# Kernel tuning notes

Hardware: AMD Instinct MI355X
Metric: run time of the kernel (lower is better)

Reference implementation:

```python
import jax, jax.numpy as jnp
import numpy as np

N, K, IN, OUT, H = 20000, 32, 128, 256, 64  # H = OUT // 4 (bottleneck hidden)
EPS = 1e-5

def leaky(x):
    return jnp.where(x >= 0, x, 0.1 * x)

def bn(x, g, b, axes):
    # training-mode batch norm: batch statistics over `axes`, per-channel affine
    m = jnp.mean(x, axis=axes, keepdims=True)
    v = jnp.var(x, axis=axes, keepdims=True)
    return (x - m) * jax.lax.rsqrt(v + EPS) * g + b

def setup_inputs() -> dict:
    key = jax.random.key(0)
    ks = jax.random.split(key, 12)
    q_pts = jax.random.normal(ks[0], (N, 3), jnp.float32)
    return {
        'features': jax.random.normal(ks[1], (N, IN), jnp.float32),
        'q_pts': q_pts,
        's_pts': q_pts,  # non-strided block: queries == supports
        'neighb_inds': jax.random.randint(ks[2], (N, K), 0, N, dtype=jnp.int32),
        'w_unary1': jax.random.normal(ks[3], (IN, H), jnp.float32) * 0.05,
        'g1': jnp.ones(H, jnp.float32), 'b1': jnp.zeros(H, jnp.float32),
        'w_conv0': jax.random.normal(ks[4], (H, H), jnp.float32) * 0.05,
        'g_bn0': jnp.ones(H, jnp.float32), 'b_bn0': jnp.zeros(H, jnp.float32),
        'w_conv1': jax.random.normal(ks[5], (H, H * 3), jnp.float32) * 0.05,
        'g_bn1': jnp.ones(H, jnp.float32), 'b_bn1': jnp.zeros(H, jnp.float32),
        'g_bnc': jnp.ones(H, jnp.float32), 'b_bnc': jnp.zeros(H, jnp.float32),
        'w_unary2': jax.random.normal(ks[6], (H, OUT), jnp.float32) * 0.05,
        'g2': jnp.ones(OUT, jnp.float32), 'b2': jnp.zeros(OUT, jnp.float32),
        'w_sc': jax.random.normal(ks[7], (IN, OUT), jnp.float32) * 0.05,
        'g_sc': jnp.ones(OUT, jnp.float32), 'b_sc': jnp.zeros(OUT, jnp.float32),
    }

def reference(features, q_pts, s_pts, neighb_inds,
              w_unary1, g1, b1,
              w_conv0, g_bn0, b_bn0,
              w_conv1, g_bn1, b_bn1,
              g_bnc, b_bnc,
              w_unary2, g2, b2,
              w_sc, g_sc, b_sc):
    # unary1: Linear -> BN1d -> LeakyReLU
    x = leaky(bn(features @ w_unary1, g1, b1, 0))              # [N, H]
    # pad with zero shadow row (index N = out-of-range neighbor)
    s_pad = jnp.concatenate([s_pts, jnp.zeros((1, 3), s_pts.dtype)], 0)
    f_pad = jnp.concatenate([x, jnp.zeros((1, H), x.dtype)], 0)
    nb_x = s_pad[neighb_inds] - q_pts[:, None, :]              # [N, K, 3]
    nb_y = f_pad[neighb_inds]                                  # [N, K, H]
    # adaptive kernel generation: 1x1 conv -> BN2d -> LeakyReLU -> 1x1 conv
    k0 = leaky(bn(jnp.einsum('nkc,cd->nkd', nb_y, w_conv0), g_bn0, b_bn0, (0, 1)))
    kern = jnp.einsum('nkd,de->nke', k0, w_conv1).reshape(N, K, H, 3)
    # per-neighbor dynamic matmul: [H,3] @ [3] per (n,k)
    msg = jnp.einsum('nkhc,nkc->nkh', kern, nb_x)              # [N, K, H]
    msg = leaky(bn(msg, g_bn1, b_bn1, (0, 1)))
    agg = jnp.max(msg, axis=1)                                 # [N, H] max over neighbors
    # batch_norm_conv + LeakyReLU
    agg = leaky(bn(agg, g_bnc, b_bnc, 0))
    # unary2 (no relu) + shortcut (no relu)
    xo = bn(agg @ w_unary2, g2, b2, 0)                         # [N, OUT]
    sc = bn(features @ w_sc, g_sc, b_sc, 0)                    # [N, OUT]
    return leaky(xo + sc)
```

## Files before the change

kernel.cpp:

```cpp
#include <hip/hip_runtime.h>

#define KNB 32
#define CIN 128
#define CH 64
#define COUT 256
#define BN_EPS 1e-5f
#define CONV_GRID 256

typedef __attribute__((ext_vector_type(8))) short bf16x8;
typedef __attribute__((ext_vector_type(4))) float f32x4;

static __device__ __forceinline__ float leakyf(float v){ return fmaxf(v, 0.1f*v); }

static __device__ __forceinline__ unsigned short f2bf(float f){
    unsigned u = __float_as_uint(f);
    u += 0x7FFFu + ((u >> 16) & 1u);
    return (unsigned short)(u >> 16);
}
static __device__ __forceinline__ float bf2f(ushort u){ return __uint_as_float(((unsigned)u) << 16); }

static __device__ __forceinline__ unsigned cvtpk(float lo, float hi){
    unsigned r;
    asm("v_cvt_pk_bf16_f32 %0, %1, %2" : "=v"(r) : "v"(lo), "v"(hi));
    return r;
}

static __device__ __forceinline__ void bn_affine_wave(const float* __restrict__ G, const float* __restrict__ s,
    const float* __restrict__ W, const float* __restrict__ gg, const float* __restrict__ bb,
    float invcnt, int D, int M, int o, int lane, float& ai, float& ci)
{
    float pm = 0.f, pq = 0.f;
    for (int i = lane; i < D; i += 64){
        float wi = W[i*M + o];
        pm += s[i]*wi;
        float t = 0.f;
        for (int j = 0; j < D; ++j) t += G[i*D + j]*W[j*M + o];
        pq += wi*t;
    }
    #pragma unroll
    for (int off = 32; off; off >>= 1){
        pm += __shfl_down(pm, off);
        pq += __shfl_down(pq, off);
    }
    float m  = pm*invcnt;
    float var = pq*invcnt - m*m;
    float a_ = gg[o]*rsqrtf(var + BN_EPS);
    float c_ = bb[o] - m*a_;
    ai = __shfl(a_, 0);
    ci = __shfl(c_, 0);
}

__global__ __launch_bounds__(512) void k1_kernel(const float* __restrict__ feat, const int* __restrict__ inds,
    const float* __restrict__ W1, int N,
    float* __restrict__ slabA, ushort* __restrict__ featbf, ushort* __restrict__ w1s,
    ushort* __restrict__ xbf, float* __restrict__ cnt)
{
    __shared__ ushort Xt[128][40];
    __shared__ float red[16][128];
    int tid = threadIdx.x, bid = blockIdx.x;
    if (bid < 128){
        int wave = tid >> 6, lane = tid & 63, l15 = lane & 15, g = lane >> 4;
        int wr = wave >> 1, wc = wave & 1;
        const f32x4 z4 = {0.f,0.f,0.f,0.f};
        f32x4 acc[2][4];
        #pragma unroll
        for (int i=0;i<2;++i)
            #pragma unroll
            for (int j=0;j<4;++j) acc[i][j] = z4;
        float pcs[4] = {0,0,0,0};
        int nch = (N + 31) >> 5;
        for (int ch = bid; ch < nch; ch += 128){
            int base = ch << 5;
            __syncthreads();
            #pragma unroll
            for (int ii=0; ii<2; ++ii){
                int i = tid + ii*512;
                int r = i >> 5, c4 = i & 31;
                int n = base + r;
                float4 v = make_float4(0.f,0.f,0.f,0.f);
                if (n < N) v = ((const float4*)feat)[(size_t)n*32 + c4];
                ushort b0=f2bf(v.x), b1=f2bf(v.y), b2=f2bf(v.z), b3=f2bf(v.w);
                Xt[c4*4+0][r]=b0; Xt[c4*4+1][r]=b1; Xt[c4*4+2][r]=b2; Xt[c4*4+3][r]=b3;
                pcs[0]+=bf2f(b0); pcs[1]+=bf2f(b1); pcs[2]+=bf2f(b2); pcs[3]+=bf2f(b3);
            }
            __syncthreads();
            bf16x8 af[2], bv[4];
            #pragma unroll
            for (int t=0;t<2;++t) af[t] = *(const bf16x8*)&Xt[wr*32 + t*16 + l15][g*8];
            #pragma unroll
            for (int u=0;u<4;++u) bv[u] = *(const bf16x8*)&Xt[wc*64 + u*16 + l15][g*8];
            #pragma unroll
            for (int t=0;t<2;++t)
                #pragma unroll
                for (int u=0;u<4;++u)
                    acc[t][u] = __builtin_amdgcn_mfma_f32_16x16x32_bf16(af[t], bv[u], acc[t][u], 0,0,0);
        }
        float* Gp = slabA + (size_t)bid*16512;
        #pragma unroll
        for (int t=0;t<2;++t)
            #pragma unroll
            for (int u=0;u<4;++u)
                #pragma unroll
                for (int q=0;q<4;++q)
                    Gp[(wr*32 + t*16 + g*4 + q)*CIN + wc*64 + u*16 + l15] = acc[t][u][q];
        __syncthreads();
        { int r16 = tid >> 5, c4 = tid & 31;
          #pragma unroll
          for (int j=0;j<4;++j) red[r16][c4*4+j] = pcs[j]; }
        __syncthreads();
        if (tid < CIN){
            float s = 0.f;
            #pragma unroll
            for (int k=0;k<16;++k) s += red[k][tid];
            Gp[16384 + tid] = s;
        }
    } else {
        int t2 = (bid-128)*512 + tid;
        const int TG = 128*512;
        for (int i = t2; i < N*32; i += TG){
            float4 v = ((const float4*)feat)[i];
            uint2 pk; pk.x = cvtpk(v.x, v.y); pk.y = cvtpk(v.z, v.w);
            ((uint2*)featbf)[i] = pk;
        }
        for (int i = t2; i < N*KNB; i += TG){
            int ix = inds[i];
            if ((unsigned)ix < (unsigned)N) atomicAdd(&cnt[ix], 1.0f);
        }
        if (t2 < 192*CH){
            int r = t2 >> 6, dd = t2 & 63;
            int c = r >> 6, h = r & 63;
            w1s[t2] = f2bf(W1[dd*192 + 3*h + c]);
        }
        if (t2 < CH) xbf[(size_t)N*CH + t2] = 0;
    }
}

__global__ __launch_bounds__(256) void reduce_slab(const float* __restrict__ slab, int nparts, int len,
                                                   float* __restrict__ dst)
{
    int j = blockIdx.x*256 + threadIdx.x;
    if (j < len){
        float s0 = 0.f, s1 = 0.f, s2 = 0.f, s3 = 0.f;
        int b = 0;
        for (; b + 4 <= nparts; b += 4){
            s0 += slab[(size_t)(b+0)*len + j];
            s1 += slab[(size_t)(b+1)*len + j];
            s2 += slab[(size_t)(b+2)*len + j];
            s3 += slab[(size_t)(b+3)*len + j];
        }
        for (; b < nparts; ++b) s0 += slab[(size_t)b*len + j];
        dst[j] = (s0 + s1) + (s2 + s3);
    }
}

__global__ __launch_bounds__(512) void k3_finA(const float* __restrict__ XtX, const float* __restrict__ fsum,
    const float* __restrict__ Wu1, const float* __restrict__ g1, const float* __restrict__ b1,
    const float* __restrict__ Wsc, const float* __restrict__ gsc, const float* __restrict__ bsc,
    float invN, float* __restrict__ c1v, ushort* __restrict__ w1t,
    ushort* __restrict__ wcat, float* __restrict__ cscv)
{
    int gw = blockIdx.x*8 + (threadIdx.x >> 6), lane = threadIdx.x & 63;
    if (gw < 64){
        int o = gw; float ai, ci;
        bn_affine_wave(XtX, fsum, Wu1, g1, b1, invN, CIN, CH, o, lane, ai, ci);
        if (lane == 0) c1v[o] = ci;
        for (int k = lane; k < CIN; k += 64) w1t[o*CIN + k] = f2bf(ai*Wu1[k*CH + o]);
    } else if (gw < 320){
        int o = gw - 64; float ai, ci;
        bn_affine_wave(XtX, fsum, Wsc, gsc, bsc, invN, CIN, COUT, o, lane, ai, ci);
        if (lane == 0) cscv[o] = ci;
        for (int k = lane; k < CIN; k += 64) wcat[o*192 + k] = f2bf(ai*Wsc[k*COUT + o]);
    }
}

__global__ __launch_bounds__(512) void k4_unary1_gram(const ushort* __restrict__ featbf,
    const ushort* __restrict__ w1t, const float* __restrict__ c1v, const float* __restrict__ cnt,
    ushort* __restrict__ xbf, float* __restrict__ slabB, int N)
{
    __shared__ ushort Xp[64][136];
    __shared__ ushort Xw[64][136];
    __shared__ float red[8][64];
    int tid = threadIdx.x, bid = blockIdx.x;
    int wave = tid >> 6, lane = tid & 63, l15 = lane & 15, g = lane >> 4;
    const f32x4 z4 = {0.f,0.f,0.f,0.f};
    int row0 = bid*128 + wave*16;
    f32x4 acc[4] = {z4, z4, z4, z4};
    int r = row0 + l15;
    bool ok = r < N;
    #pragma unroll
    for (int s=0;s<4;++s){
        bf16x8 af = {0,0,0,0,0,0,0,0};
        if (ok) af = *(const bf16x8*)(featbf + (size_t)r*CIN + s*32 + g*8);
        #pragma unroll
        for (int nt=0;nt<4;++nt){
            bf16x8 bfr = *(const bf16x8*)(w1t + (size_t)(nt*16+l15)*CIN + s*32 + g*8);
            acc[nt] = __builtin_amdgcn_mfma_f32_16x16x32_bf16(af, bfr, acc[nt], 0,0,0);
        }
    }
    float wq[4];
    #pragma unroll
    for (int q=0;q<4;++q){
        int rr = row0 + g*4 + q;
        wq[q] = (rr < N) ? cnt[rr] : 0.f;
    }
    float ps[4] = {0,0,0,0};
    #pragma unroll
    for (int nt=0;nt<4;++nt){
        int col = nt*16 + l15;
        float cc = c1v[col];
        #pragma unroll
        for (int q=0;q<4;++q){
            int rr = row0 + g*4 + q;
            int lr = wave*16 + g*4 + q;
            float v = (rr < N) ? leakyf(acc[nt][q] + cc) : 0.f;
            ushort b = f2bf(v);
            if (rr < N) xbf[(size_t)rr*CH + col] = b;
            Xp[col][lr] = b;
            float wv = wq[q]*v;
            Xw[col][lr] = f2bf(wv);
            ps[nt] += wv;
        }
    }
    #pragma unroll
    for (int nt=0;nt<4;++nt){
        ps[nt] += __shfl_xor(ps[nt], 16);
        ps[nt] += __shfl_xor(ps[nt], 32);
        if (lane < 16) red[wave][nt*16 + l15] = ps[nt];
    }
    __syncthreads();
    int mr = wave >> 1, ncb = (wave & 1)*2;
    f32x4 ac2[2] = {z4, z4};
    #pragma unroll
    for (int ks=0;ks<4;++ks){
        bf16x8 af = *(const bf16x8*)&Xw[mr*16 + l15][ks*32 + g*8];
        #pragma unroll
        for (int u=0;u<2;++u){
            bf16x8 bv = *(const bf16x8*)&Xp[(ncb+u)*16 + l15][ks*32 + g*8];
            ac2[u] = __builtin_amdgcn_mfma_f32_16x16x32_bf16(af, bv, ac2[u], 0,0,0);
        }
    }
    float* Gp = slabB + (size_t)bid*4160;
    #pragma unroll
    for (int u=0;u<2;++u)
        #pragma unroll
        for (int q=0;q<4;++q)
            Gp[(mr*16 + g*4 + q)*CH + (ncb+u)*16 + l15] = ac2[u][q];
    if (tid < CH){
        float s = 0.f;
        #pragma unroll
        for (int w8=0;w8<8;++w8) s += red[w8][tid];
        Gp[4096 + tid] = s;
    }
}

__global__ __launch_bounds__(512) void conv_msg_mfma(
    const ushort* __restrict__ xbf, const float* __restrict__ qp, const float* __restrict__ sp,
    const int* __restrict__ inds, const ushort* __restrict__ w1s,
    const float* __restrict__ G0, const float* __restrict__ s0,
    const float* __restrict__ W0, const float* __restrict__ gb0, const float* __restrict__ bb0,
    float* __restrict__ mx, float* __restrict__ mn, float* __restrict__ msgpart, int N)
{
    __shared__ unsigned char SM[24576 + 8*12288];
    __shared__ float a0s[64], c0s[64];
    int tid = threadIdx.x, bid = blockIdx.x;
    int warp = tid >> 6, lane = tid & 63;
    int l15 = lane & 15, g = lane >> 4;
    for (int ch = tid; ch < 1536; ch += 512){
        int r = ch >> 3, c16 = ch & 7;
        uint4 v = ((const uint4*)w1s)[ch];
        *(uint4*)(SM + r*128 + ((c16*16) ^ ((r&7)<<4))) = v;
    }
    float invNK = 1.0f/((float)N*KNB);
    #pragma unroll
    for (int j=0;j<8;++j){
        int o = warp*8 + j;
        float ai, ci;
        bn_affine_wave(G0, s0, W0, gb0, bb0, invNK, CH, CH, o, lane, ai, ci);
        if (lane == 0){ a0s[o] = ai; c0s[o] = ci; }
    }
    __syncthreads();
    bf16x8 wf[8];
    #pragma unroll
    for (int mt=0;mt<4;++mt){
        int d = mt*16 + l15;
        float ad = a0s[d];
        #pragma unroll
        for (int s=0;s<2;++s){
            bf16x8 t;
            #pragma unroll
            for (int j=0;j<8;++j) t[j] = (short)f2bf(ad*W0[(s*32 + g*8 + j)*CH + d]);
            wf[mt*2+s] = t;
        }
    }
    float c0r[16];
    #pragma unroll
    for (int mt=0;mt<4;++mt)
        #pragma unroll
        for (int q=0;q<4;++q)
            c0r[mt*4+q] = c0s[mt*16 + g*4 + q];
    unsigned char* k0base = SM + 24576 + warp*12288;
    unsigned swz = (unsigned)((l15 & 7) << 4);
    float ps[4] = {0,0,0,0}, pss[4] = {0,0,0,0};
    const f32x4 z4 = {0.f,0.f,0.f,0.f};

    for (int n = bid*8 + warp; n < N; n += CONV_GRID*8){
        int ix0 = inds[n*KNB + l15];
        int ix1 = inds[n*KNB + 16 + l15];
        if ((unsigned)ix0 > (unsigned)N) ix0 = N;
        if ((unsigned)ix1 > (unsigned)N) ix1 = N;
        float qx = qp[n*3+0], qy = qp[n*3+1], qz = qp[n*3+2];
        float nbv[2][3];
        if (ix0 < N){ nbv[0][0]=sp[ix0*3]-qx; nbv[0][1]=sp[ix0*3+1]-qy; nbv[0][2]=sp[ix0*3+2]-qz; }
        else        { nbv[0][0]=-qx; nbv[0][1]=-qy; nbv[0][2]=-qz; }
        if (ix1 < N){ nbv[1][0]=sp[ix1*3]-qx; nbv[1][1]=sp[ix1*3+1]-qy; nbv[1][2]=sp[ix1*3+2]-qz; }
        else        { nbv[1][0]=-qx; nbv[1][1]=-qy; nbv[1][2]=-qz; }
        bf16x8 xf0a = *(const bf16x8*)(xbf + (size_t)ix0*CH +      g*8);
        bf16x8 xf0b = *(const bf16x8*)(xbf + (size_t)ix0*CH + 32 + g*8);
        bf16x8 xf1a = *(const bf16x8*)(xbf + (size_t)ix1*CH +      g*8);
        bf16x8 xf1b = *(const bf16x8*)(xbf + (size_t)ix1*CH + 32 + g*8);
        f32x4 acc0[8];
        #pragma unroll
        for (int i=0;i<8;++i) acc0[i] = z4;
        #pragma unroll
        for (int mt=0;mt<4;++mt){
            acc0[mt*2+0] = __builtin_amdgcn_mfma_f32_16x16x32_bf16(wf[mt*2+0], xf0a, acc0[mt*2+0], 0,0,0);
            acc0[mt*2+0] = __builtin_amdgcn_mfma_f32_16x16x32_bf16(wf[mt*2+1], xf0b, acc0[mt*2+0], 0,0,0);
            acc0[mt*2+1] = __builtin_amdgcn_mfma_f32_16x16x32_bf16(wf[mt*2+0], xf1a, acc0[mt*2+1], 0,0,0);
            acc0[mt*2+1] = __builtin_amdgcn_mfma_f32_16x16x32_bf16(wf[mt*2+1], xf1b, acc0[mt*2+1], 0,0,0);
        }
        #pragma unroll
        for (int mt=0;mt<4;++mt){
            #pragma unroll
            for (int ntk=0;ntk<2;++ntk){
                f32x4 a = acc0[mt*2+ntk];
                float v0 = leakyf(a[0] + c0r[mt*4+0]);
                float v1 = leakyf(a[1] + c0r[mt*4+1]);
                float v2 = leakyf(a[2] + c0r[mt*4+2]);
                float v3 = leakyf(a[3] + c0r[mt*4+3]);
                #pragma unroll
                for (int c=0;c<3;++c){
                    float w = nbv[ntk][c];
                    uint2 pk;
                    pk.x = cvtpk(v0*w, v1*w);
                    pk.y = cvtpk(v2*w, v3*w);
                    *(uint2*)(k0base + (c*32 + ntk*16 + l15)*128 + ((unsigned)(mt*32 + g*8) ^ swz)) = pk;
                }
            }
        }
        f32x4 acc1[8];
        #pragma unroll
        for (int i=0;i<8;++i) acc1[i] = z4;
        #pragma unroll
        for (int c=0;c<3;++c){
            #pragma unroll
            for (int ks=0;ks<2;++ks){
                unsigned co = ((unsigned)(ks*64 + g*16)) ^ swz;
                bf16x8 a0f = *(const bf16x8*)(k0base + (c*32 +      l15)*128 + co);
                bf16x8 a1f = *(const bf16x8*)(k0base + (c*32 + 16 + l15)*128 + co);
                #pragma unroll
                for (int nt=0;nt<4;++nt){
                    bf16x8 bfr = *(const bf16x8*)(SM + (c*64 + nt*16 + l15)*128 + co);
                    acc1[0*4+nt] = __builtin_amdgcn_mfma_f32_16x16x32_bf16(a0f, bfr, acc1[0*4+nt], 0,0,0);
                    acc1[1*4+nt] = __builtin_amdgcn_mfma_f32_16x16x32_bf16(a1f, bfr, acc1[1*4+nt], 0,0,0);
                }
            }
        }
        #pragma unroll
        for (int nt=0;nt<4;++nt){
            float vmx = -3.4e38f, vmn = 3.4e38f, s = 0.f, ssq = 0.f;
            #pragma unroll
            for (int mtk=0;mtk<2;++mtk){
                f32x4 a = acc1[mtk*4+nt];
                #pragma unroll
                for (int q=0;q<4;++q){
                    float v = a[q];
                    vmx = fmaxf(vmx, v); vmn = fminf(vmn, v);
                    s += v; ssq += v*v;
                }
            }
            vmx = fmaxf(vmx, __shfl_xor(vmx, 16)); vmn = fminf(vmn, __shfl_xor(vmn, 16));
            s  += __shfl_xor(s, 16);               ssq += __shfl_xor(ssq, 16);
            vmx = fmaxf(vmx, __shfl_xor(vmx, 32)); vmn = fminf(vmn, __shfl_xor(vmn, 32));
            s  += __shfl_xor(s, 32);               ssq += __shfl_xor(ssq, 32);
            if (lane < 16){
                mx[(size_t)n*CH + nt*16 + l15] = vmx;
                mn[(size_t)n*CH + nt*16 + l15] = vmn;
                ps[nt] += s; pss[nt] += ssq;
            }
        }
    }
    __syncthreads();
    float* red = (float*)SM;
    if (lane < 16){
        #pragma unroll
        for (int nt=0;nt<4;++nt){
            red[warp*128 + nt*16 + l15]        = ps[nt];
            red[1024 + warp*128 + nt*16 + l15] = pss[nt];
        }
    }
    __syncthreads();
    if (tid < 64){
        float s = 0.f, ssq = 0.f;
        #pragma unroll
        for (int w8=0;w8<8;++w8){ s += red[w8*128 + tid]; ssq += red[1024 + w8*128 + tid]; }
        msgpart[(size_t)bid*128 + tid]      = s;
        msgpart[(size_t)bid*128 + 64 + tid] = ssq;
    }
}

__global__ __launch_bounds__(512) void k7_agg(const float* __restrict__ mxb, const float* __restrict__ mnb,
    const float* __restrict__ msgpart, const float* __restrict__ gb1, const float* __restrict__ bb1,
    float* __restrict__ aggb, float* __restrict__ aggpart, int N)
{
    __shared__ float r1[512], r2[512];
    __shared__ float a1ms[64], c1ms[64];
    int tid = threadIdx.x, bid = blockIdx.x;
    {
        int t = tid & 63, seg = tid >> 6;
        float s = 0.f, ss = 0.f;
        for (int r = seg; r < CONV_GRID; r += 8){ s += msgpart[r*128 + t]; ss += msgpart[r*128 + 64 + t]; }
        r1[tid] = s; r2[tid] = ss;
    }
    __syncthreads();
    if (tid < 64){
        float S = 0.f, SS = 0.f;
        #pragma unroll
        for (int k=0;k<8;++k){ S += r1[tid + 64*k]; SS += r2[tid + 64*k]; }
        float invc = 1.0f/((float)N*KNB);
        float m = S*invc, var = SS*invc - m*m;
        float ai = gb1[tid]*rsqrtf(var + BN_EPS);
        a1ms[tid] = ai; c1ms[tid] = bb1[tid] - m*ai;
    }
    __syncthreads();
    int h = tid & 63;
    float ah = a1ms[h], chh = c1ms[h];
    bool useMax = (ah >= 0.f);
    float ps = 0.f, pss = 0.f;
    for (int i = bid*512 + tid; i < N*CH; i += gridDim.x*512){
        float sel = useMax ? mxb[i] : mnb[i];
        float v = leakyf(ah*sel + chh);
        aggb[i] = v; ps += v; pss += v*v;
    }
    __syncthreads();
    r1[tid] = ps; r2[tid] = pss;
    __syncthreads();
    if (tid < 64){
        float S = 0.f, SS = 0.f;
        #pragma unroll
        for (int k=0;k<8;++k){ S += r1[tid + 64*k]; SS += r2[tid + 64*k]; }
        aggpart[(size_t)bid*128 + tid]      = S;
        aggpart[(size_t)bid*128 + 64 + tid] = SS;
    }
}

__global__ __launch_bounds__(512) void k8_gram64t(const float* __restrict__ aggb, const float* __restrict__ aggpart,
    const float* __restrict__ gbc, const float* __restrict__ bbc,
    ushort* __restrict__ a2b2, float* __restrict__ slabC, int N)
{
    __shared__ ushort Xt[64][72];
    __shared__ float red[32][64];
    __shared__ float abncs[64], cbncs[64];
    int tid = threadIdx.x, bid = blockIdx.x;
    int wave = tid >> 6, lane = tid & 63, l15 = lane & 15, g = lane >> 4;
    const f32x4 z4 = {0.f,0.f,0.f,0.f};
    {
        float* r1 = &red[0][0]; float* r2 = r1 + 512;
        int t = tid & 63, seg = tid >> 6;
        float s = 0.f, ss = 0.f;
        for (int r = seg; r < 256; r += 8){ s += aggpart[r*128 + t]; ss += aggpart[r*128 + 64 + t]; }
        r1[tid] = s; r2[tid] = ss;
        __syncthreads();
        if (tid < 64){
            float S = 0.f, SS = 0.f;
            #pragma unroll
            for (int k=0;k<8;++k){ S += r1[tid + 64*k]; SS += r2[tid + 64*k]; }
            float invc = 1.0f/(float)N;
            float m = S*invc, var = SS*invc - m*m;
            float ai = gbc[tid]*rsqrtf(var + BN_EPS);
            abncs[tid] = ai; cbncs[tid] = bbc[tid] - m*ai;
        }
        __syncthreads();
    }
    int wr = wave >> 1, wc = wave & 1;
    f32x4 acc[2] = {z4, z4};
    float pcs[4] = {0,0,0,0};
    int nch = (N + 63) >> 6;
    for (int ch = bid; ch < nch; ch += 256){
        int base = ch << 6;
        __syncthreads();
        #pragma unroll
        for (int ii=0;ii<2;++ii){
            int i = tid + ii*512;
            int r = i >> 4, cq = i & 15;
            int n = base + r;
            float4 v = make_float4(0.f,0.f,0.f,0.f);
            if (n < N){
                v = ((const float4*)aggb)[(size_t)n*16 + cq];
                v.x = leakyf(abncs[cq*4+0]*v.x + cbncs[cq*4+0]);
                v.y = leakyf(abncs[cq*4+1]*v.y + cbncs[cq*4+1]);
                v.z = leakyf(abncs[cq*4+2]*v.z + cbncs[cq*4+2]);
                v.w = leakyf(abncs[cq*4+3]*v.w + cbncs[cq*4+3]);
            }
            uint2 pk; pk.x = cvtpk(v.x, v.y); pk.y = cvtpk(v.z, v.w);
            if (n < N) ((uint2*)a2b2)[(size_t)n*16 + cq] = pk;
            Xt[cq*4+0][r] = (ushort)(pk.x & 0xffff);
            Xt[cq*4+1][r] = (ushort)(pk.x >> 16);
            Xt[cq*4+2][r] = (ushort)(pk.y & 0xffff);
            Xt[cq*4+3][r] = (ushort)(pk.y >> 16);
            pcs[0] += v.x; pcs[1] += v.y; pcs[2] += v.z; pcs[3] += v.w;
        }
        __syncthreads();
        #pragma unroll
        for (int ks=0;ks<2;++ks){
            bf16x8 af = *(const bf16x8*)&Xt[wr*16 + l15][ks*32 + g*8];
            #pragma unroll
            for (int u=0;u<2;++u){
                bf16x8 bv = *(const bf16x8*)&Xt[wc*32 + u*16 + l15][ks*32 + g*8];
                acc[u] = __builtin_amdgcn_mfma_f32_16x16x32_bf16(af, bv, acc[u], 0,0,0);
            }
        }
    }
    float* Gp = slabC + (size_t)bid*4160;
    #pragma unroll
    for (int u=0;u<2;++u)
        #pragma unroll
        for (int q=0;q<4;++q)
            Gp[(wr*16 + g*4 + q)*CH + wc*32 + u*16 + l15] = acc[u][q];
    __syncthreads();
    { int r = tid >> 4, cq = tid & 15;
      #pragma unroll
      for (int j=0;j<4;++j) red[r][cq*4+j] = pcs[j]; }
    __syncthreads();
    if (tid < CH){
        float s = 0.f;
        #pragma unroll
        for (int k=0;k<32;++k) s += red[k][tid];
        Gp[4096 + tid] = s;
    }
}

__global__ __launch_bounds__(512) void k10_fin2(const float* __restrict__ G2, const float* __restrict__ s2,
    const float* __restrict__ Wu2, const float* __restrict__ g2, const float* __restrict__ b2,
    const float* __restrict__ cscv, float invN, ushort* __restrict__ wcat, float* __restrict__ ccomb)
{
    int gw = blockIdx.x*8 + (threadIdx.x >> 6), lane = threadIdx.x & 63;
    if (gw < 256){
        float ai, ci;
        bn_affine_wave(G2, s2, Wu2, g2, b2, invN, CH, COUT, gw, lane, ai, ci);
        wcat[gw*192 + 128 + lane] = f2bf(ai*Wu2[lane*COUT + gw]);
        if (lane == 0) ccomb[gw] = cscv[gw] + ci;
    }
}

__global__ __launch_bounds__(512) void final_mfma_kernel(
    const ushort* __restrict__ featbf, const ushort* __restrict__ a2b2,
    const ushort* __restrict__ wcat, const float* __restrict__ ccomb,
    float* __restrict__ out, int N)
{
    int tid = threadIdx.x, wave = tid >> 6, lane = tid & 63;
    int l15 = lane & 15, g = lane >> 4;
    int row0 = blockIdx.x*128 + wave*16;
    const f32x4 z4 = {0.f,0.f,0.f,0.f};
    f32x4 acc[16];
    #pragma unroll
    for (int i=0;i<16;++i) acc[i] = z4;
    int r = row0 + l15;
    bool ok = r < N;
    #pragma unroll
    for (int s=0;s<6;++s){
        bf16x8 af = {0,0,0,0,0,0,0,0};
        if (ok){
            const ushort* srcp = (s < 4) ? (featbf + (size_t)r*CIN + s*32 + g*8)
                                         : (a2b2  + (size_t)r*CH + (s-4)*32 + g*8);
            af = *(const bf16x8*)srcp;
        }
        #pragma unroll
        for (int nt=0;nt<16;++nt){
            bf16x8 bfr = *(const bf16x8*)(wcat + (nt*16+l15)*192 + s*32 + g*8);
            acc[nt] = __builtin_amdgcn_mfma_f32_16x16x32_bf16(af, bfr, acc[nt], 0,0,0);
        }
    }
    #pragma unroll
    for (int nt=0;nt<16;++nt){
        float cc = ccomb[nt*16 + l15];
        #pragma unroll
        for (int q=0;q<4;++q){
            int rr = row0 + g*4 + q;
            if (rr < N) out[(size_t)rr*COUT + nt*16 + l15] = leakyf(acc[nt][q] + cc);
        }
    }
}

extern "C" void kernel_launch(void* const* d_in, const int* in_sizes, int n_in,
                              void* d_out, int out_size, void* d_ws, size_t ws_size,
                              hipStream_t stream)
{
    const float* feat = (const float*)d_in[0];
    const float* qp   = (const float*)d_in[1];
    const float* sp   = (const float*)d_in[2];
    const int*   inds = (const int*)d_in[3];
    const float* Wu1  = (const float*)d_in[4];
    const float* g1   = (const float*)d_in[5];
    const float* b1   = (const float*)d_in[6];
    const float* W0   = (const float*)d_in[7];
    const float* gb0  = (const float*)d_in[8];
    const float* bb0  = (const float*)d_in[9];
    const float* W1   = (const float*)d_in[10];
    const float* gb1  = (const float*)d_in[11];
    const float* bb1  = (const float*)d_in[12];
    const float* gbc  = (const float*)d_in[13];
    const float* bbc  = (const float*)d_in[14];
    const float* Wu2  = (const float*)d_in[15];
    const float* g2   = (const float*)d_in[16];
    const float* b2   = (const float*)d_in[17];
    const float* Wsc  = (const float*)d_in[18];
    const float* gsc  = (const float*)d_in[19];
    const float* bsc  = (const float*)d_in[20];

    const int N = in_sizes[0] / CIN;

    float* ws   = (float*)d_ws;
    float* XtX  = ws;
    float* fsum = ws + 16384;
    float* G0   = ws + 16512;
    float* s0   = G0 + 4096;
    float* G2   = ws + 16512 + 4160;
    float* s2   = G2 + 4096;
    float* cnt  = ws + 16512 + 8320;
    float* prm  = cnt + N;
    float* c1v  = prm + 64;
    float* cscv = prm + 768;
    float* msgpart = prm + 1536;
    float* aggpart = msgpart + 256*128;
    float* mxb  = aggpart + 256*128;
    float* mnb  = mxb + (size_t)N*CH;
    float* aggb = mnb + (size_t)N*CH;
    ushort* xbf    = (ushort*)(aggb + (size_t)N*CH);
    ushort* featbf = xbf + (size_t)(N+1)*CH;
    ushort* a2b2   = featbf + (size_t)N*CIN;
    ushort* w1s    = a2b2 + (size_t)N*CH;
    ushort* wcat   = w1s + 192*CH;
    ushort* w1t    = wcat + COUT*192;
    float*  ccomb  = (float*)(w1t + CH*CIN);

    float* slabA = mxb;
    float* slabB = aggb;
    float* slabC = mxb;

    const int nTiles = (N + 127)/128;

    hipMemsetAsync(cnt, 0, (size_t)N*sizeof(float), stream);
    k1_kernel<<<256, 512, 0, stream>>>(feat, inds, W1, N, slabA, featbf, w1s, xbf, cnt);
    reduce_slab<<<(16512 + 255)/256, 256, 0, stream>>>(slabA, 128, 16512, XtX);
    k3_finA<<<40, 512, 0, stream>>>(XtX, fsum, Wu1, g1, b1, Wsc, gsc, bsc, 1.0f/N, c1v, w1t, wcat, cscv);
    k4_unary1_gram<<<nTiles, 512, 0, stream>>>(featbf, w1t, c1v, cnt, xbf, slabB, N);
    reduce_slab<<<(4160 + 255)/256, 256, 0, stream>>>(slabB, nTiles, 4160, G0);
    conv_msg_mfma<<<CONV_GRID, 512, 0, stream>>>(xbf, qp, sp, inds, w1s, G0, s0, W0, gb0, bb0, mxb, mnb, msgpart, N);
    k7_agg<<<256, 512, 0, stream>>>(mxb, mnb, msgpart, gb1, bb1, aggb, aggpart, N);
    k8_gram64t<<<256, 512, 0, stream>>>(aggb, aggpart, gbc, bbc, a2b2, slabC, N);
    reduce_slab<<<(4160 + 255)/256, 256, 0, stream>>>(slabC, 256, 4160, G2);
    k10_fin2<<<32, 512, 0, stream>>>(G2, s2, Wu2, g2, b2, cscv, 1.0f/N, wcat, ccomb);
    final_mfma_kernel<<<nTiles, 512, 0, stream>>>(featbf, a2b2, wcat, ccomb, (float*)d_out, N);
}
```

Measured before the change: 274.3 us.

## Fuse BN2 affine finalization into final GEMM and stage scaled weights in LDS

Removes the k10_fin2 launch by having every block of the final GEMM recompute the BN affine parameters for unary2 from the Gram matrix. The scaled Wu2 tile is built in shared memory and read from there. The conv kernel's scaled W0 fragments are also staged through a transposed LDS tile instead of strided global loads, and the Gram loop index order is swapped so the inner loop reads G by column. The cost is that each of ~157 final blocks redundantly runs 256 wave-level 64x64 quadratic-form reductions before starting its GEMM.

```diff
diff --git a/kernel.cpp b/kernel.cpp
--- a/kernel.cpp
+++ b/kernel.cpp
@@ -30,12 +30,12 @@
     float invcnt, int D, int M, int o, int lane, float& ai, float& ci)
 {
     float pm = 0.f, pq = 0.f;
-    for (int i = lane; i < D; i += 64){
-        float wi = W[i*M + o];
-        pm += s[i]*wi;
+    for (int j = lane; j < D; j += 64){
+        float wj = W[j*M + o];
+        pm += s[j]*wj;
         float t = 0.f;
-        for (int j = 0; j < D; ++j) t += G[i*D + j]*W[j*M + o];
-        pq += wi*t;
+        for (int i = 0; i < D; ++i) t += G[i*D + j]*W[i*M + o];
+        pq += wj*t;
     }
     #pragma unroll
     for (int off = 32; off; off >>= 1){
@@ -262,6 +262,7 @@
 {
     __shared__ unsigned char SM[24576 + 8*12288];
     __shared__ float a0s[64], c0s[64];
+    __shared__ ushort w0tl[64*72];
     int tid = threadIdx.x, bid = blockIdx.x;
     int warp = tid >> 6, lane = tid & 63;
     int l15 = lane & 15, g = lane >> 4;
@@ -270,28 +271,28 @@
         uint4 v = ((const uint4*)w1s)[ch];
         *(uint4*)(SM + r*128 + ((c16*16) ^ ((r&7)<<4))) = v;
     }
-    float invNK = 1.0f/((float)N*KNB);
-    #pragma unroll
-    for (int j=0;j<8;++j){
-        int o = warp*8 + j;
-        float ai, ci;
-        bn_affine_wave(G0, s0, W0, gb0, bb0, invNK, CH, CH, o, lane, ai, ci);
-        if (lane == 0){ a0s[o] = ai; c0s[o] = ci; }
+    {
+        float invNK = 1.0f/((float)N*KNB);
+        #pragma unroll
+        for (int rr = 0; rr < 8; ++rr){
+            int o = warp*8 + rr;
+            float ai, ci;
+            bn_affine_wave(G0, s0, W0, gb0, bb0, invNK, CH, CH, o, lane, ai, ci);
+            if (lane == 0){ a0s[o] = ai; c0s[o] = ci; }
+        }
+    }
+    __syncthreads();
+    for (int i = tid; i < 4096; i += 512){
+        int c = i >> 6, d = i & 63;
+        w0tl[d*72 + c] = f2bf(a0s[d]*W0[i]);
     }
     __syncthreads();
     bf16x8 wf[8];
     #pragma unroll
-    for (int mt=0;mt<4;++mt){
-        int d = mt*16 + l15;
-        float ad = a0s[d];
-        #pragma unroll
-        for (int s=0;s<2;++s){
-            bf16x8 t;
-            #pragma unroll
-            for (int j=0;j<8;++j) t[j] = (short)f2bf(ad*W0[(s*32 + g*8 + j)*CH + d]);
-            wf[mt*2+s] = t;
-        }
-    }
+    for (int mt=0;mt<4;++mt)
+        #pragma unroll
+        for (int s=0;s<2;++s)
+            wf[mt*2+s] = *(const bf16x8*)&w0tl[(mt*16+l15)*72 + s*32 + g*8];
     float c0r[16];
     #pragma unroll
     for (int mt=0;mt<4;++mt)
@@ -302,6 +303,7 @@
     unsigned swz = (unsigned)((l15 & 7) << 4);
     float ps[4] = {0,0,0,0}, pss[4] = {0,0,0,0};
     const f32x4 z4 = {0.f,0.f,0.f,0.f};
+    __syncthreads();
 
     for (int n = bid*8 + warp; n < N; n += CONV_GRID*8){
         int ix0 = inds[n*KNB + l15];
@@ -539,26 +541,31 @@
     }
 }
 
-__global__ __launch_bounds__(512) void k10_fin2(const float* __restrict__ G2, const float* __restrict__ s2,
-    const float* __restrict__ Wu2, const float* __restrict__ g2, const float* __restrict__ b2,
-    const float* __restrict__ cscv, float invN, ushort* __restrict__ wcat, float* __restrict__ ccomb)
-{
-    int gw = blockIdx.x*8 + (threadIdx.x >> 6), lane = threadIdx.x & 63;
-    if (gw < 256){
-        float ai, ci;
-        bn_affine_wave(G2, s2, Wu2, g2, b2, invN, CH, COUT, gw, lane, ai, ci);
-        wcat[gw*192 + 128 + lane] = f2bf(ai*Wu2[lane*COUT + gw]);
-        if (lane == 0) ccomb[gw] = cscv[gw] + ci;
-    }
-}
-
 __global__ __launch_bounds__(512) void final_mfma_kernel(
     const ushort* __restrict__ featbf, const ushort* __restrict__ a2b2,
-    const ushort* __restrict__ wcat, const float* __restrict__ ccomb,
+    const ushort* __restrict__ wcat,
+    const float* __restrict__ G2, const float* __restrict__ s2,
+    const float* __restrict__ Wu2, const float* __restrict__ g2, const float* __restrict__ b2,
+    const float* __restrict__ cscv, float invN,
     float* __restrict__ out, int N)
 {
+    __shared__ ushort wu2tl[256*72];
+    __shared__ float a2s[256], ccl[256];
     int tid = threadIdx.x, wave = tid >> 6, lane = tid & 63;
     int l15 = lane & 15, g = lane >> 4;
+    for (int rep = 0; rep < 32; ++rep){
+        int o = wave*32 + rep;
+        float ai, ci;
+        bn_affine_wave(G2, s2, Wu2, g2, b2, invN, CH, COUT, o, lane, ai, ci);
+        if (lane == 0){ a2s[o] = ai; ccl[o] = cscv[o] + ci; }
+    }
+    __syncthreads();
+    for (int i = tid; i < 64*256; i += 512){
+        int k = i >> 8, o = i & 255;
+        wu2tl[o*72 + k] = f2bf(a2s[o]*Wu2[i]);
+    }
+    __syncthreads();
+
     int row0 = blockIdx.x*128 + wave*16;
     const f32x4 z4 = {0.f,0.f,0.f,0.f};
     f32x4 acc[16];
@@ -576,13 +583,15 @@
         }
         #pragma unroll
         for (int nt=0;nt<16;++nt){
-            bf16x8 bfr = *(const bf16x8*)(wcat + (nt*16+l15)*192 + s*32 + g*8);
+            bf16x8 bfr;
+            if (s < 4) bfr = *(const bf16x8*)(wcat + (size_t)(nt*16+l15)*192 + s*32 + g*8);
+            else       bfr = *(const bf16x8*)&wu2tl[(nt*16+l15)*72 + (s-4)*32 + g*8];
             acc[nt] = __builtin_amdgcn_mfma_f32_16x16x32_bf16(af, bfr, acc[nt], 0,0,0);
         }
     }
     #pragma unroll
     for (int nt=0;nt<16;++nt){
-        float cc = ccomb[nt*16 + l15];
+        float cc = ccl[nt*16 + l15];
         #pragma unroll
         for (int q=0;q<4;++q){
             int rr = row0 + g*4 + q;
@@ -631,7 +640,7 @@
     float* c1v  = prm + 64;
     float* cscv = prm + 768;
     float* msgpart = prm + 1536;
-    float* aggpart = msgpart + 256*128;
+    float* aggpart = msgpart + CONV_GRID*128;
     float* mxb  = aggpart + 256*128;
     float* mnb  = mxb + (size_t)N*CH;
     float* aggb = mnb + (size_t)N*CH;
@@ -641,7 +650,6 @@
     ushort* w1s    = a2b2 + (size_t)N*CH;
     ushort* wcat   = w1s + 192*CH;
     ushort* w1t    = wcat + COUT*192;
-    float*  ccomb  = (float*)(w1t + CH*CIN);
 
     float* slabA = mxb;
     float* slabB = aggb;
@@ -659,6 +667,5 @@
     k7_agg<<<256, 512, 0, stream>>>(mxb, mnb, msgpart, gb1, bb1, aggb, aggpart, N);
     k8_gram64t<<<256, 512, 0, stream>>>(aggb, aggpart, gbc, bbc, a2b2, slabC, N);
     reduce_slab<<<(4160 + 255)/256, 256, 0, stream>>>(slabC, 256, 4160, G2);
-    k10_fin2<<<32, 512, 0, stream>>>(G2, s2, Wu2, g2, b2, cscv, 1.0f/N, wcat, ccomb);
-    final_mfma_kernel<<<nTiles, 512, 0, stream>>>(featbf, a2b2, wcat, ccomb, (float*)d_out, N);
-}
+    final_mfma_kernel<<<nTiles, 512, 0, stream>>>(featbf, a2b2, wcat, G2, s2, Wu2, g2, b2, cscv, 1.0f/N, (float*)d_out, N);
+}
```

New measurement: 305.9 us. +11.5%, slower.
